# Kernel optimization log

Hardware: AMD Instinct MI355X
Metric: run time of the kernel (lower is better)

The kernel has to match this reference:

```python
import jax, jax.numpy as jnp
import numpy as np

MAX_FREQ = 4
OMEGA = 0.5 * np.pi
PATCH = 64


def _unnorm(c, size):
    # align_corners=False convention of torch.grid_sample
    return ((c + 1.0) * size - 1.0) / 2.0


def _gather(im, yy, xx):
    # im [C,H,W], yy/xx [Ho,Wo] -> [C,Ho,Wo]
    return im[:, yy, xx]


def _gs_nearest(inp, grid):
    # inp [B,C,H,W], grid [B,Ho,Wo,2] (x,y); padding_mode='border'
    B, C, H, W = inp.shape
    x = jnp.clip(jnp.round(_unnorm(grid[..., 0], W)), 0, W - 1).astype(jnp.int32)
    y = jnp.clip(jnp.round(_unnorm(grid[..., 1], H)), 0, H - 1).astype(jnp.int32)
    return jax.vmap(_gather)(inp, y, x)  # [B,C,Ho,Wo]


def _gs_bilinear(inp, grid):
    B, C, H, W = inp.shape
    x = jnp.clip(_unnorm(grid[..., 0], W), 0.0, W - 1.0)
    y = jnp.clip(_unnorm(grid[..., 1], H), 0.0, H - 1.0)
    x0 = jnp.floor(x); y0 = jnp.floor(y)
    wx = (x - x0)[:, None]; wy = (y - y0)[:, None]  # [B,1,Ho,Wo]
    x0i = x0.astype(jnp.int32); y0i = y0.astype(jnp.int32)
    x1i = jnp.minimum(x0i + 1, W - 1); y1i = jnp.minimum(y0i + 1, H - 1)
    g = jax.vmap(_gather)
    v00 = g(inp, y0i, x0i); v01 = g(inp, y0i, x1i)
    v10 = g(inp, y1i, x0i); v11 = g(inp, y1i, x1i)
    return (v00 * (1 - wx) * (1 - wy) + v01 * wx * (1 - wy)
            + v10 * (1 - wx) * wy + v11 * wx * wy)


def _conv2d(x, w, b):
    y = jax.lax.conv_general_dilated(x, w, (1, 1), ((1, 1), (1, 1)),
                                     dimension_numbers=("NCHW", "OIHW", "NCHW"))
    return y + b[None, :, None, None]


def _lc_decoder(q, rel):
    # q [B,Ho,Wo,2F+1], rel [B,Ho,Wo,1]; Fourier basis [1, cos(k*w*rel), sin(k*w*rel)]
    k = jnp.arange(1, MAX_FREQ + 1, dtype=q.dtype)
    ang = rel * k * OMEGA  # [B,Ho,Wo,F]
    basis = jnp.concatenate([jnp.ones_like(rel), jnp.cos(ang), jnp.sin(ang)], axis=-1)
    return jnp.sum(q * basis, axis=-1, keepdims=True)  # [B,Ho,Wo,1]


def _forward(sinogram, feat, grid, square_inv, adapt_w, adapt_b):
    B = feat.shape[0]
    sino = _conv2d(feat, adapt_w, adapt_b)          # [B,2F+1,V,D]
    V, D = sino.shape[-2], sino.shape[-1]
    # make_coord along detector axis (dim=1 coord channel), padding=0
    coord_d = ((jnp.arange(D, dtype=sino.dtype) + 0.5) / D) * 2.0 - 1.0
    sino_coord = jnp.broadcast_to(coord_d[None, None, None, :], (B, 1, V, D))
    shift_interval = 1.0 / D
    eps = 1e-4
    q_recons, lengths = [], []
    for sx in (-shift_interval, shift_interval):  # ensembling shifts
        g = grid + jnp.array([sx, 0.0], dtype=grid.dtype) + 1e-6
        q_recon = jnp.transpose(_gs_nearest(sino, g), (0, 2, 3, 1))       # [B,V,P2,2F+1]
        q_coord = jnp.transpose(_gs_nearest(sino_coord, g), (0, 2, 3, 1))  # [B,V,P2,1]
        rel = (grid[..., 0:1] - q_coord) * D
        q_recons.append(_lc_decoder(q_recon, rel))
        lengths.append(jnp.abs(rel) + eps)
    tot = lengths[0] + lengths[1]
    # lengths are swapped before weighting (cross weighting)
    recon = q_recons[0] * lengths[1] / tot + q_recons[1] * lengths[0] / tot
    out = jnp.sum(jnp.transpose(recon, (0, 3, 1, 2)) * square_inv * 10000.0, axis=-2)
    # back projection of center channel of raw sinogram
    ch = sinogram.shape[1]
    bp = _gs_bilinear(sinogram[:, ch // 2:ch // 2 + 1], grid)
    out = out + jnp.sum(bp * square_inv * 10000.0, axis=-2)  # [B,1,P2]
    return out.reshape(B, 1, PATCH, PATCH)


def setup_inputs() -> dict:
    key = jax.random.key(0)
    ks = jax.random.split(key, 6)
    B, V, D, ENC = 4, 360, 512, 64
    P2 = PATCH * PATCH
    CH = 2 * MAX_FREQ + 1
    return {
        "sinogram": jax.random.normal(ks[0], (B, 1, V, D), jnp.float32),
        "feat": jax.random.normal(ks[1], (B, ENC, V, D), jnp.float32),
        "grid": jax.random.uniform(ks[2], (B, V, P2, 2), jnp.float32, -1.0, 1.0),
        "square_inv": jax.random.uniform(ks[3], (B, 1, V, P2), jnp.float32, 1e-5, 1e-4),
        "adapt_w": jax.random.normal(ks[4], (CH, ENC, 3, 3), jnp.float32) * 0.05,
        "adapt_b": jax.random.normal(ks[5], (CH,), jnp.float32) * 0.05,
    }


def reference(sinogram, feat, grid, square_inv, adapt_w, adapt_b):
    return _forward(sinogram, feat, grid, square_inv, adapt_w, adapt_b)
```

## Files before the change

### kernel.cpp

```cpp
#include <hip/hip_runtime.h>
#include <hip/hip_fp16.h>
#include <math.h>

#define B   4
#define V   360
#define D   512
#define ENC 64
#define CH  9
#define P2  4096
#define NCHUNK 90
#define VCHUNK 4
#define RECH 16
#define PENT 513
#define PENTB 64

template <int PAIR>
__global__ __launch_bounds__(64) void conv_kernel(
    const float* __restrict__ feat,
    const float* __restrict__ w,
    const float* __restrict__ bias,
    char* __restrict__ outp)
{
    const int bid = blockIdx.x;
    const int sw  = (bid & 7) * 180 + (bid >> 3);
    const int b   = sw / V;
    const int v   = sw % V;
    const int d0  = threadIdx.x * 8;

    float acc[CH][8];
    #pragma unroll
    for (int oc = 0; oc < CH; ++oc) {
        const float bv = bias[oc];
        #pragma unroll
        for (int p = 0; p < 8; ++p) acc[oc][p] = bv;
    }

    const float* fb = feat + ((size_t)b * ENC * V + v) * D + d0;
    const bool vm = v > 0, vp = v < V - 1;
    const bool dm = d0 > 0, dp = d0 + 8 < D;

    float r0[3][10], r1[3][10];

    auto ld = [&](float r[3][10], int ic) {
        const float* f = fb + (size_t)ic * (V * D);
        #pragma unroll
        for (int rr = 0; rr < 3; ++rr) {
            const float* fr = f + (rr - 1) * D;
            const bool ok = (rr == 0) ? vm : ((rr == 2) ? vp : true);
            float4 c0 = ok ? *(const float4*)fr       : float4{0.f, 0.f, 0.f, 0.f};
            float4 c1 = ok ? *(const float4*)(fr + 4) : float4{0.f, 0.f, 0.f, 0.f};
            r[rr][1] = c0.x; r[rr][2] = c0.y; r[rr][3] = c0.z; r[rr][4] = c0.w;
            r[rr][5] = c1.x; r[rr][6] = c1.y; r[rr][7] = c1.z; r[rr][8] = c1.w;
            r[rr][0] = (ok && dm) ? fr[-1] : 0.f;
            r[rr][9] = (ok && dp) ? fr[8]  : 0.f;
        }
    };
    auto fmab = [&](const float r[3][10], int ic) {
        #pragma unroll
        for (int oc = 0; oc < CH; ++oc) {
            const float* ww = w + ((size_t)oc * ENC + ic) * 9;
            #pragma unroll
            for (int kr = 0; kr < 3; ++kr) {
                #pragma unroll
                for (int kc = 0; kc < 3; ++kc) {
                    const float wv = ww[kr * 3 + kc];
                    #pragma unroll
                    for (int p = 0; p < 8; ++p)
                        acc[oc][p] = fmaf(r[kr][p + kc], wv, acc[oc][p]);
                }
            }
        }
    };

    ld(r0, 0);
    #pragma unroll 1
    for (int ic = 0; ic < ENC; ic += 2) {
        ld(r1, ic + 1);
        fmab(r0, ic);
        if (ic + 2 < ENC) ld(r0, ic + 2);
        fmab(r1, ic + 1);
    }

    #pragma unroll
    for (int p = 0; p < 8; ++p) {
        union { __half2 h; unsigned u; } cv;
        uint4 pk;
        cv.h = __floats2half2_rn(acc[0][p], acc[1][p]); pk.x = cv.u;
        cv.h = __floats2half2_rn(acc[2][p], acc[3][p]); pk.y = cv.u;
        cv.h = __floats2half2_rn(acc[4][p], acc[5][p]); pk.z = cv.u;
        cv.h = __floats2half2_rn(acc[6][p], acc[7][p]); pk.w = cv.u;
        cv.h = __floats2half2_rn(acc[8][p], 0.f);
        const unsigned short z = (unsigned short)(cv.u & 0xffffu);
        const int x = d0 + p;
        if (PAIR) {
            char* row = outp + (size_t)(b * V + v) * PENT * PENTB;
            char* eA = row + (size_t)(x + 1) * PENTB;
            *(uint4*)eA = pk;
            *(unsigned short*)(eA + 32) = z;
            char* eB = row + (size_t)x * PENTB + 16;
            *(uint4*)eB = pk;
            *(unsigned short*)(eB + 18) = z;
            if (x == 0) {
                *(uint4*)row = pk;
                *(unsigned short*)(row + 32) = z;
            }
            if (x == D - 1) {
                char* eC = row + (size_t)512 * PENTB + 16;
                *(uint4*)eC = pk;
                *(unsigned short*)(eC + 18) = z;
            }
        } else {
            __half* rec = (__half*)outp + (size_t)(((size_t)b * V + v) * D + x) * RECH;
            *(uint4*)rec = pk;
            *(unsigned*)(rec + 8) = (unsigned)z;
        }
    }
}

__global__ __launch_bounds__(256) void build_sg4(
    const float* __restrict__ sg, float4* __restrict__ sg4)
{
    const int i  = blockIdx.x * 256 + threadIdx.x;
    const int x  = i & (D - 1);
    const int bv = i >> 9;
    const int v  = bv % V;
    const float a = sg[i];
    const float c = (x < D - 1) ? sg[i + 1] : a;
    const int i2 = (v < V - 1) ? i + D : i;
    const float d2 = sg[i2];
    const float e2 = (x < D - 1) ? sg[i2 + 1] : d2;
    sg4[i] = float4{a, c, d2, e2};
}

__global__ __launch_bounds__(256) void build_sg2(
    const float* __restrict__ sg, float2* __restrict__ sg2)
{
    const int i = blockIdx.x * 256 + threadIdx.x;
    const int x = i & (D - 1);
    const float a = sg[i];
    const float c = (x == D - 1) ? a : sg[i + 1];
    sg2[i] = float2{a, c};
}

__device__ __forceinline__ float decode_rec(uint4 a, unsigned short z, float rel)
{
    float q[9];
    union { unsigned uu; __half2 h; } c;
    float2 f;
    c.uu = a.x; f = __half22float2(c.h); q[0] = f.x; q[1] = f.y;
    c.uu = a.y; f = __half22float2(c.h); q[2] = f.x; q[3] = f.y;
    c.uu = a.z; f = __half22float2(c.h); q[4] = f.x; q[5] = f.y;
    c.uu = a.w; f = __half22float2(c.h); q[6] = f.x; q[7] = f.y;
    union { unsigned short us; __half hh; } c2;
    c2.us = z;
    q[8] = __half2float(c2.hh);

    const float ang = rel * 1.5707963267948966f;
    float s1, c1;
    __sincosf(ang, &s1, &c1);
    const float c2f = fmaf(2.f * c1, c1, -1.f);
    const float s2f = 2.f * c1 * s1;
    const float c3f = fmaf(2.f * c1, c2f, -c1);
    const float s3f = fmaf(2.f * c1, s2f, -s1);
    const float c4f = fmaf(2.f * c1, c3f, -c2f);
    const float s4f = fmaf(2.f * c1, s3f, -s2f);

    float vv = q[0];
    vv = fmaf(q[1], c1,  vv); vv = fmaf(q[2], c2f, vv);
    vv = fmaf(q[3], c3f, vv); vv = fmaf(q[4], c4f, vv);
    vv = fmaf(q[5], s1,  vv); vv = fmaf(q[6], s2f, vv);
    vv = fmaf(q[7], s3f, vv); vv = fmaf(q[8], s4f, vv);
    return vv;
}

template <int SG4>
__global__ __launch_bounds__(256) void sample_pair(
    const char* __restrict__ pair,
    const float4* __restrict__ sg4,
    const float2* __restrict__ sg2,
    const float* __restrict__ grid,
    const float* __restrict__ sq,
    float* __restrict__ partial)
{
    const int bid = blockIdx.x;
    const int xcd = bid & 7;
    const int b   = xcd >> 1;
    const int idx = ((bid >> 3) << 1) | (xcd & 1);
    const int chunk = idx >> 4;
    const int p  = (idx & 15) * 256 + threadIdx.x;
    const int v0 = chunk * VCHUNK;

    const char*   pb  = pair + (size_t)b * V * PENT * PENTB;
    const float4* s4b = sg4 + (size_t)b * V * D;
    const float2* s2b = sg2 + (size_t)b * V * D;

    float gx[4], gy[4], sv[4];
    #pragma unroll
    for (int u = 0; u < 4; ++u) {
        const size_t gi = (size_t)(b * V + v0 + u) * P2 + p;
        const double gd = __builtin_nontemporal_load((const double*)grid + gi);
        const unsigned long long gu = __double_as_longlong(gd);
        gx[u] = __uint_as_float((unsigned)gu);
        gy[u] = __uint_as_float((unsigned)(gu >> 32));
        sv[u] = __builtin_nontemporal_load(sq + gi);
    }

    uint4 qa[4], qb[4];
    unsigned short zA[4], zB[4];
    float relm[4], relp[4];
    #pragma unroll
    for (int u = 0; u < 4; ++u) {
        const float fy = ((gy[u] + 1e-6f + 1.f) * (float)V - 1.f) * 0.5f;
        const int   yi = (int)fminf(fmaxf(rintf(fy), 0.f), (float)(V - 1));
        const float fx0 = ((gx[u] + 1e-6f + 1.f) * (float)D - 1.f) * 0.5f;
        const int xm = (int)fminf(fmaxf(rintf(fx0 - 0.5f), 0.f), (float)(D - 1));
        const int xp = (int)fminf(fmaxf(rintf(fx0 + 0.5f), 0.f), (float)(D - 1));
        const float qcm = ((float)xm + 0.5f) * (2.f / (float)D) - 1.f;
        const float qcp = ((float)xp + 0.5f) * (2.f / (float)D) - 1.f;
        relm[u] = (gx[u] - qcm) * (float)D;
        relp[u] = (gx[u] - qcp) * (float)D;
        const char* rowp = pb + (size_t)yi * (PENT * PENTB);
        const char* e1 = rowp + (size_t)(xm + 1) * PENTB;
        const char* e2 = rowp + (size_t)xp * PENTB;
        qa[u] = *(const uint4*)e1;
        qb[u] = *(const uint4*)(e2 + 16);
        const unsigned zab = *(const unsigned*)(e1 + 32);
        zA[u] = (unsigned short)(zab & 0xffffu);
        zB[u] = (e2 == e1) ? (unsigned short)(zab >> 16)
                           : *(const unsigned short*)(e2 + 34);
    }

    float bl00[4], bl01[4], bl10[4], bl11[4], wxv[4], wyv[4];
    #pragma unroll
    for (int u = 0; u < 4; ++u) {
        float fxb = fminf(fmaxf(((gx[u] + 1.f) * (float)D - 1.f) * 0.5f, 0.f), (float)(D - 1));
        float fyb = fminf(fmaxf(((gy[u] + 1.f) * (float)V - 1.f) * 0.5f, 0.f), (float)(V - 1));
        const float x0 = floorf(fxb), y0 = floorf(fyb);
        wxv[u] = fxb - x0; wyv[u] = fyb - y0;
        const int x0i = (int)x0, y0i = (int)y0;
        if (SG4) {
            const float4 t = s4b[y0i * D + x0i];
            bl00[u] = t.x; bl01[u] = t.y; bl10[u] = t.z; bl11[u] = t.w;
        } else {
            const int y1i = min(y0i + 1, V - 1);
            const float2 t  = s2b[y0i * D + x0i];
            const float2 u2 = s2b[y1i * D + x0i];
            bl00[u] = t.x;  bl01[u] = t.y;
            bl10[u] = u2.x; bl11[u] = u2.y;
        }
    }

    __builtin_amdgcn_sched_barrier(0);

    float acc = 0.f;
    #pragma unroll
    for (int u = 0; u < 4; ++u) {
        const float vmv = decode_rec(qa[u], zA[u], relm[u]);
        const float vpv = decode_rec(qb[u], zB[u], relp[u]);
        const float lm = fabsf(relm[u]) + 1e-4f;
        const float lp = fabsf(relp[u]) + 1e-4f;
        const float recon = (vmv * lp + vpv * lm) / (lm + lp);

        const float wx = wxv[u], wy = wyv[u];
        const float bp = bl00[u] * (1.f - wx) * (1.f - wy) + bl01[u] * wx * (1.f - wy)
                       + bl10[u] * (1.f - wx) * wy         + bl11[u] * wx * wy;

        acc += (recon + bp) * sv[u] * 1e4f;
    }
    __builtin_nontemporal_store(acc, partial + ((size_t)chunk * B + b) * P2 + p);
}

template <int PAIRED>
__global__ __launch_bounds__(256) void sample_basic(
    const __half* __restrict__ sino,
    const float* __restrict__ sinogram,
    const float2* __restrict__ sg2,
    const float* __restrict__ grid,
    const float* __restrict__ sq,
    float* __restrict__ partial)
{
    const int bid = blockIdx.x;
    const int xcd = bid & 7;
    const int b   = xcd >> 1;
    const int idx = ((bid >> 3) << 1) | (xcd & 1);
    const int chunk = idx >> 4;
    const int p  = (idx & 15) * 256 + threadIdx.x;
    const int v0 = chunk * VCHUNK;

    const float*  sg   = sinogram + (size_t)b * V * D;
    const float2* s2b  = sg2 + (size_t)b * V * D;
    const __half* sb   = sino + (size_t)b * V * D * RECH;

    float gx[4], gy[4], sv[4];
    #pragma unroll
    for (int u = 0; u < 4; ++u) {
        const size_t gi = (size_t)(b * V + v0 + u) * P2 + p;
        const double gd = __builtin_nontemporal_load((const double*)grid + gi);
        const unsigned long long gu = __double_as_longlong(gd);
        gx[u] = __uint_as_float((unsigned)gu);
        gy[u] = __uint_as_float((unsigned)(gu >> 32));
        sv[u] = __builtin_nontemporal_load(sq + gi);
    }

    uint4    ra[4][2];
    unsigned rz[4][2];
    float    rel[4][2];
    #pragma unroll
    for (int u = 0; u < 4; ++u) {
        const float fy = ((gy[u] + 1e-6f + 1.f) * (float)V - 1.f) * 0.5f;
        const int   yi = (int)fminf(fmaxf(rintf(fy), 0.f), (float)(V - 1));
        const float fx0 = ((gx[u] + 1e-6f + 1.f) * (float)D - 1.f) * 0.5f;
        #pragma unroll
        for (int sft = 0; sft < 2; ++sft) {
            const float fx = (sft == 0) ? (fx0 - 0.5f) : (fx0 + 0.5f);
            const int   xi = (int)fminf(fmaxf(rintf(fx), 0.f), (float)(D - 1));
            const float qc = ((float)xi + 0.5f) * (2.f / (float)D) - 1.f;
            rel[u][sft] = (gx[u] - qc) * (float)D;
            const __half* rec = sb + (size_t)(yi * D + xi) * RECH;
            ra[u][sft] = *(const uint4*)rec;
            rz[u][sft] = *(const unsigned*)(rec + 8);
        }
    }

    float bl00[4], bl01[4], bl10[4], bl11[4], wxv[4], wyv[4];
    #pragma unroll
    for (int u = 0; u < 4; ++u) {
        float fxb = fminf(fmaxf(((gx[u] + 1.f) * (float)D - 1.f) * 0.5f, 0.f), (float)(D - 1));
        float fyb = fminf(fmaxf(((gy[u] + 1.f) * (float)V - 1.f) * 0.5f, 0.f), (float)(V - 1));
        const float x0 = floorf(fxb), y0 = floorf(fyb);
        wxv[u] = fxb - x0; wyv[u] = fyb - y0;
        const int x0i = (int)x0, y0i = (int)y0;
        const int y1i = min(y0i + 1, V - 1);
        if (PAIRED) {
            const float2 t  = s2b[y0i * D + x0i];
            const float2 u2 = s2b[y1i * D + x0i];
            bl00[u] = t.x;  bl01[u] = t.y;
            bl10[u] = u2.x; bl11[u] = u2.y;
        } else {
            const int x1i = min(x0i + 1, D - 1);
            bl00[u] = sg[y0i * D + x0i]; bl01[u] = sg[y0i * D + x1i];
            bl10[u] = sg[y1i * D + x0i]; bl11[u] = sg[y1i * D + x1i];
        }
    }

    __builtin_amdgcn_sched_barrier(0);

    float acc = 0.f;
    #pragma unroll
    for (int u = 0; u < 4; ++u) {
        const float v0f = decode_rec(ra[u][0], (unsigned short)(rz[u][0] & 0xffffu), rel[u][0]);
        const float v1f = decode_rec(ra[u][1], (unsigned short)(rz[u][1] & 0xffffu), rel[u][1]);
        const float l0 = fabsf(rel[u][0]) + 1e-4f;
        const float l1 = fabsf(rel[u][1]) + 1e-4f;
        const float recon = (v0f * l1 + v1f * l0) / (l0 + l1);
        const float wx = wxv[u], wy = wyv[u];
        const float bp = bl00[u] * (1.f - wx) * (1.f - wy) + bl01[u] * wx * (1.f - wy)
                       + bl10[u] * (1.f - wx) * wy         + bl11[u] * wx * wy;
        acc += (recon + bp) * sv[u] * 1e4f;
    }
    __builtin_nontemporal_store(acc, partial + ((size_t)chunk * B + b) * P2 + p);
}

__global__ __launch_bounds__(256) void reduce_kernel(
    const float* __restrict__ partial, float* __restrict__ out)
{
    const int i = blockIdx.x * 256 + threadIdx.x;
    float a = 0.f;
    #pragma unroll 6
    for (int c = 0; c < NCHUNK; ++c)
        a += __builtin_nontemporal_load(partial + (size_t)c * B * P2 + i);
    out[i] = a;
}

extern "C" void kernel_launch(void* const* d_in, const int* in_sizes, int n_in,
                              void* d_out, int out_size, void* d_ws, size_t ws_size,
                              hipStream_t stream)
{
    const float* sinogram = (const float*)d_in[0];
    const float* feat     = (const float*)d_in[1];
    const float* grid     = (const float*)d_in[2];
    const float* sq       = (const float*)d_in[3];
    const float* w        = (const float*)d_in[4];
    const float* bias     = (const float*)d_in[5];
    float* out = (float*)d_out;

    const size_t pair_b = (size_t)B * V * PENT * PENTB;
    const size_t part_b = (size_t)NCHUNK * B * P2 * sizeof(float);
    const size_t sg4_b  = (size_t)B * V * D * sizeof(float4);
    const size_t sg2_b  = (size_t)B * V * D * sizeof(float2);
    const size_t rec_b  = (size_t)B * V * D * RECH * sizeof(__half);

    if (ws_size >= pair_b + part_b + sg4_b) {
        char*   pair    = (char*)d_ws;
        float*  partial = (float*)((char*)d_ws + pair_b);
        float4* sg4     = (float4*)((char*)d_ws + pair_b + part_b);
        conv_kernel<1><<<dim3(1440), 64, 0, stream>>>(feat, w, bias, pair);
        build_sg4<<<dim3(2880), 256, 0, stream>>>(sinogram, sg4);
        sample_pair<1><<<dim3(5760), 256, 0, stream>>>(pair, sg4, (const float2*)sg4, grid, sq, partial);
        reduce_kernel<<<dim3((B * P2) / 256), 256, 0, stream>>>(partial, out);
    } else if (ws_size >= pair_b + part_b + sg2_b) {
        char*   pair    = (char*)d_ws;
        float*  partial = (float*)((char*)d_ws + pair_b);
        float2* sg2     = (float2*)((char*)d_ws + pair_b + part_b);
        conv_kernel<1><<<dim3(1440), 64, 0, stream>>>(feat, w, bias, pair);
        build_sg2<<<dim3(2880), 256, 0, stream>>>(sinogram, sg2);
        sample_pair<0><<<dim3(5760), 256, 0, stream>>>(pair, (const float4*)sg2, sg2, grid, sq, partial);
        reduce_kernel<<<dim3((B * P2) / 256), 256, 0, stream>>>(partial, out);
    } else if (ws_size >= rec_b + part_b + sg2_b) {
        char*   sino    = (char*)d_ws;
        float*  partial = (float*)((char*)d_ws + rec_b);
        float2* sg2     = (float2*)((char*)d_ws + rec_b + part_b);
        conv_kernel<0><<<dim3(1440), 64, 0, stream>>>(feat, w, bias, sino);
        build_sg2<<<dim3(2880), 256, 0, stream>>>(sinogram, sg2);
        sample_basic<1><<<dim3(5760), 256, 0, stream>>>((const __half*)sino, sinogram, sg2, grid, sq, partial);
        reduce_kernel<<<dim3((B * P2) / 256), 256, 0, stream>>>(partial, out);
    } else {
        char*   sino    = (char*)d_ws;
        float*  partial = (float*)((char*)d_ws + rec_b);
        conv_kernel<0><<<dim3(1440), 64, 0, stream>>>(feat, w, bias, sino);
        sample_basic<0><<<dim3(5760), 256, 0, stream>>>((const __half*)sino, sinogram, (const float2*)sino, grid, sq, partial);
        reduce_kernel<<<dim3((B * P2) / 256), 256, 0, stream>>>(partial, out);
    }
}
```

Before: 330.1 us.

## Use packed fp16 dot2 for conv with prepacked half2 weights and larger blocks

Converts the 3x3 conv inner loop from fp32 FMAs to v_dot2 on half2 pairs of input channels, and adds a small kernel that packs the weights into half2 per channel pair. Blocks grow from 64 to 256 threads covering four view rows, and the grid shrinks to match. The aim is to halve the conv's FMA instruction count. In exchange it loses precision on the inputs and weights, drops the software double-buffered loads, and adds one extra kernel launch.

```diff
diff --git a/kernel.cpp b/kernel.cpp
--- a/kernel.cpp
+++ b/kernel.cpp
@@ -13,19 +13,55 @@
 #define RECH 16
 #define PENT 513
 #define PENTB 64
+#define NIC2 (ENC / 2)
+#define WPN  (NIC2 * CH * 9)
+
+typedef _Float16 hp2 __attribute__((ext_vector_type(2)));
+
+__device__ __forceinline__ float dot2f(unsigned a, unsigned b, float c)
+{
+#if __has_builtin(__builtin_amdgcn_fdot2)
+    return __builtin_amdgcn_fdot2(__builtin_bit_cast(hp2, a),
+                                  __builtin_bit_cast(hp2, b), c, false);
+#else
+    union { unsigned u; __half2 h; } ua, ub;
+    ua.u = a; ub.u = b;
+    const float2 fa = __half22float2(ua.h);
+    const float2 fb = __half22float2(ub.h);
+    return fmaf(fa.y, fb.y, fmaf(fa.x, fb.x, c));
+#endif
+}
+
+__global__ __launch_bounds__(256) void pack_weights(
+    const float* __restrict__ w, unsigned* __restrict__ wp)
+{
+    const int i = blockIdx.x * 256 + threadIdx.x;
+    if (i >= WPN) return;
+    const int ic2 = i / (CH * 9);
+    const int r   = i - ic2 * (CH * 9);
+    const int oc  = r / 9;
+    const int k   = r - oc * 9;
+    const float a = w[((size_t)oc * ENC + 2 * ic2) * 9 + k];
+    const float b = w[((size_t)oc * ENC + 2 * ic2 + 1) * 9 + k];
+    union { __half2 h; unsigned u; } cv;
+    cv.h = __floats2half2_rn(a, b);
+    wp[i] = cv.u;
+}
 
 template <int PAIR>
-__global__ __launch_bounds__(64) void conv_kernel(
+__global__ __launch_bounds__(256) void conv_kernel(
     const float* __restrict__ feat,
-    const float* __restrict__ w,
+    const unsigned* __restrict__ wp,
     const float* __restrict__ bias,
     char* __restrict__ outp)
 {
     const int bid = blockIdx.x;
-    const int sw  = (bid & 7) * 180 + (bid >> 3);
-    const int b   = sw / V;
-    const int v   = sw % V;
-    const int d0  = threadIdx.x * 8;
+    const int sw  = (bid & 7) * 45 + (bid >> 3);
+    const int b   = sw / 90;
+    const int vt  = sw % 90;
+    const int tr  = threadIdx.x >> 6;
+    const int v   = vt * 4 + tr;
+    const int d0  = (threadIdx.x & 63) * 8;
 
     float acc[CH][8];
     #pragma unroll
@@ -39,46 +75,50 @@
     const bool vm = v > 0, vp = v < V - 1;
     const bool dm = d0 > 0, dp = d0 + 8 < D;
 
-    float r0[3][10], r1[3][10];
-
-    auto ld = [&](float r[3][10], int ic) {
-        const float* f = fb + (size_t)ic * (V * D);
+    #pragma unroll 1
+    for (int ic2 = 0; ic2 < NIC2; ++ic2) {
+        float rA[3][10], rB[3][10];
         #pragma unroll
-        for (int rr = 0; rr < 3; ++rr) {
-            const float* fr = f + (rr - 1) * D;
-            const bool ok = (rr == 0) ? vm : ((rr == 2) ? vp : true);
-            float4 c0 = ok ? *(const float4*)fr       : float4{0.f, 0.f, 0.f, 0.f};
-            float4 c1 = ok ? *(const float4*)(fr + 4) : float4{0.f, 0.f, 0.f, 0.f};
-            r[rr][1] = c0.x; r[rr][2] = c0.y; r[rr][3] = c0.z; r[rr][4] = c0.w;
-            r[rr][5] = c1.x; r[rr][6] = c1.y; r[rr][7] = c1.z; r[rr][8] = c1.w;
-            r[rr][0] = (ok && dm) ? fr[-1] : 0.f;
-            r[rr][9] = (ok && dp) ? fr[8]  : 0.f;
-        }
-    };
-    auto fmab = [&](const float r[3][10], int ic) {
+        for (int half = 0; half < 2; ++half) {
+            float (*r)[10] = half ? rB : rA;
+            const float* f = fb + (size_t)(2 * ic2 + half) * (V * D);
+            #pragma unroll
+            for (int rr = 0; rr < 3; ++rr) {
+                const float* fr = f + (rr - 1) * D;
+                const bool ok = (rr == 0) ? vm : ((rr == 2) ? vp : true);
+                float4 c0 = ok ? *(const float4*)fr       : float4{0.f, 0.f, 0.f, 0.f};
+                float4 c1 = ok ? *(const float4*)(fr + 4) : float4{0.f, 0.f, 0.f, 0.f};
+                r[rr][1] = c0.x; r[rr][2] = c0.y; r[rr][3] = c0.z; r[rr][4] = c0.w;
+                r[rr][5] = c1.x; r[rr][6] = c1.y; r[rr][7] = c1.z; r[rr][8] = c1.w;
+                r[rr][0] = (ok && dm) ? fr[-1] : 0.f;
+                r[rr][9] = (ok && dp) ? fr[8]  : 0.f;
+            }
+        }
+        unsigned pv[3][10];
+        #pragma unroll
+        for (int rr = 0; rr < 3; ++rr)
+            #pragma unroll
+            for (int t = 0; t < 10; ++t) {
+                union { __half2 h; unsigned u; } cv;
+                cv.h = __floats2half2_rn(rA[rr][t], rB[rr][t]);
+                pv[rr][t] = cv.u;
+            }
+
+        const unsigned* wbase = wp + ic2 * (CH * 9);
         #pragma unroll
         for (int oc = 0; oc < CH; ++oc) {
-            const float* ww = w + ((size_t)oc * ENC + ic) * 9;
+            const unsigned* ww = wbase + oc * 9;
             #pragma unroll
             for (int kr = 0; kr < 3; ++kr) {
                 #pragma unroll
                 for (int kc = 0; kc < 3; ++kc) {
-                    const float wv = ww[kr * 3 + kc];
+                    const unsigned wv = ww[kr * 3 + kc];
                     #pragma unroll
                     for (int p = 0; p < 8; ++p)
-                        acc[oc][p] = fmaf(r[kr][p + kc], wv, acc[oc][p]);
+                        acc[oc][p] = dot2f(pv[kr][p + kc], wv, acc[oc][p]);
                 }
             }
         }
-    };
-
-    ld(r0, 0);
-    #pragma unroll 1
-    for (int ic = 0; ic < ENC; ic += 2) {
-        ld(r1, ic + 1);
-        fmab(r0, ic);
-        if (ic + 2 < ENC) ld(r0, ic + 2);
-        fmab(r1, ic + 1);
     }
 
     #pragma unroll
@@ -389,35 +429,44 @@
     const size_t sg4_b  = (size_t)B * V * D * sizeof(float4);
     const size_t sg2_b  = (size_t)B * V * D * sizeof(float2);
     const size_t rec_b  = (size_t)B * V * D * RECH * sizeof(__half);
-
-    if (ws_size >= pair_b + part_b + sg4_b) {
-        char*   pair    = (char*)d_ws;
-        float*  partial = (float*)((char*)d_ws + pair_b);
-        float4* sg4     = (float4*)((char*)d_ws + pair_b + part_b);
-        conv_kernel<1><<<dim3(1440), 64, 0, stream>>>(feat, w, bias, pair);
+    const size_t wp_b   = (size_t)WPN * sizeof(unsigned);
+
+    if (ws_size >= pair_b + part_b + sg4_b + wp_b) {
+        char*     pair    = (char*)d_ws;
+        float*    partial = (float*)((char*)d_ws + pair_b);
+        float4*   sg4     = (float4*)((char*)d_ws + pair_b + part_b);
+        unsigned* wpp     = (unsigned*)((char*)d_ws + pair_b + part_b + sg4_b);
+        pack_weights<<<dim3((WPN + 255) / 256), 256, 0, stream>>>(w, wpp);
+        conv_kernel<1><<<dim3(360), 256, 0, stream>>>(feat, wpp, bias, pair);
         build_sg4<<<dim3(2880), 256, 0, stream>>>(sinogram, sg4);
         sample_pair<1><<<dim3(5760), 256, 0, stream>>>(pair, sg4, (const float2*)sg4, grid, sq, partial);
         reduce_kernel<<<dim3((B * P2) / 256), 256, 0, stream>>>(partial, out);
-    } else if (ws_size >= pair_b + part_b + sg2_b) {
-        char*   pair    = (char*)d_ws;
-        float*  partial = (float*)((char*)d_ws + pair_b);
-        float2* sg2     = (float2*)((char*)d_ws + pair_b + part_b);
-        conv_kernel<1><<<dim3(1440), 64, 0, stream>>>(feat, w, bias, pair);
+    } else if (ws_size >= pair_b + part_b + sg2_b + wp_b) {
+        char*     pair    = (char*)d_ws;
+        float*    partial = (float*)((char*)d_ws + pair_b);
+        float2*   sg2     = (float2*)((char*)d_ws + pair_b + part_b);
+        unsigned* wpp     = (unsigned*)((char*)d_ws + pair_b + part_b + sg2_b);
+        pack_weights<<<dim3((WPN + 255) / 256), 256, 0, stream>>>(w, wpp);
+        conv_kernel<1><<<dim3(360), 256, 0, stream>>>(feat, wpp, bias, pair);
         build_sg2<<<dim3(2880), 256, 0, stream>>>(sinogram, sg2);
         sample_pair<0><<<dim3(5760), 256, 0, stream>>>(pair, (const float4*)sg2, sg2, grid, sq, partial);
         reduce_kernel<<<dim3((B * P2) / 256), 256, 0, stream>>>(partial, out);
-    } else if (ws_size >= rec_b + part_b + sg2_b) {
-        char*   sino    = (char*)d_ws;
-        float*  partial = (float*)((char*)d_ws + rec_b);
-        float2* sg2     = (float2*)((char*)d_ws + rec_b + part_b);
-        conv_kernel<0><<<dim3(1440), 64, 0, stream>>>(feat, w, bias, sino);
+    } else if (ws_size >= rec_b + part_b + sg2_b + wp_b) {
+        char*     sino    = (char*)d_ws;
+        float*    partial = (float*)((char*)d_ws + rec_b);
+        float2*   sg2     = (float2*)((char*)d_ws + rec_b + part_b);
+        unsigned* wpp     = (unsigned*)((char*)d_ws + rec_b + part_b + sg2_b);
+        pack_weights<<<dim3((WPN + 255) / 256), 256, 0, stream>>>(w, wpp);
+        conv_kernel<0><<<dim3(360), 256, 0, stream>>>(feat, wpp, bias, sino);
         build_sg2<<<dim3(2880), 256, 0, stream>>>(sinogram, sg2);
         sample_basic<1><<<dim3(5760), 256, 0, stream>>>((const __half*)sino, sinogram, sg2, grid, sq, partial);
         reduce_kernel<<<dim3((B * P2) / 256), 256, 0, stream>>>(partial, out);
     } else {
-        char*   sino    = (char*)d_ws;
-        float*  partial = (float*)((char*)d_ws + rec_b);
-        conv_kernel<0><<<dim3(1440), 64, 0, stream>>>(feat, w, bias, sino);
+        char*     sino    = (char*)d_ws;
+        float*    partial = (float*)((char*)d_ws + rec_b);
+        unsigned* wpp     = (unsigned*)((char*)d_ws + rec_b + part_b);
+        pack_weights<<<dim3((WPN + 255) / 256), 256, 0, stream>>>(w, wpp);
+        conv_kernel<0><<<dim3(360), 256, 0, stream>>>(feat, wpp, bias, sino);
         sample_basic<0><<<dim3(5760), 256, 0, stream>>>((const __half*)sino, sinogram, (const float2*)sino, grid, sq, partial);
         reduce_kernel<<<dim3((B * P2) / 256), 256, 0, stream>>>(partial, out);
     }
```

New measurement: 354.6 us. +7.4%, slower.

## Split conv over input-channel halves with a combine pass, use 256-thread blocks

Applied to the files above, without the earlier changes.

The 3x3 adapter conv is split across two halves of the input channels. Each half writes fp32 partial sums to a new workspace buffer, and a separate combine kernel adds them and packs the fp16 pair layout. Conv blocks grow from 64 to 256 threads covering four rows, and the manual double-buffered load loop is replaced by a simple loop. The aim is more parallelism and occupancy in the conv, paid for by an extra kernel launch and a round trip of about 26MB of partials through memory. The split path needs a larger workspace; otherwise it falls back to the single-pass conv.

```diff
diff --git a/kernel.cpp b/kernel.cpp
--- a/kernel.cpp
+++ b/kernel.cpp
@@ -13,19 +13,152 @@
 #define RECH 16
 #define PENT 513
 #define PENTB 64
+#define NPX (B * V * D)
+
+typedef float vfloat4 __attribute__((ext_vector_type(4)));
+
+__device__ __forceinline__ void ld_rows8(
+    float r[3][10], const float* f, bool vm, bool vp, bool dm, bool dp)
+{
+    #pragma unroll
+    for (int rr = 0; rr < 3; ++rr) {
+        const float* fr = f + (rr - 1) * D;
+        const bool ok = (rr == 0) ? vm : ((rr == 2) ? vp : true);
+        float4 c0 = ok ? *(const float4*)fr       : float4{0.f, 0.f, 0.f, 0.f};
+        float4 c1 = ok ? *(const float4*)(fr + 4) : float4{0.f, 0.f, 0.f, 0.f};
+        r[rr][1] = c0.x; r[rr][2] = c0.y; r[rr][3] = c0.z; r[rr][4] = c0.w;
+        r[rr][5] = c1.x; r[rr][6] = c1.y; r[rr][7] = c1.z; r[rr][8] = c1.w;
+        r[rr][0] = (ok && dm) ? fr[-1] : 0.f;
+        r[rr][9] = (ok && dp) ? fr[8]  : 0.f;
+    }
+}
+
+__device__ __forceinline__ void fma_block8(
+    float acc[CH][8], const float r[3][10], const float* __restrict__ w, int ic)
+{
+    #pragma unroll
+    for (int oc = 0; oc < CH; ++oc) {
+        const float* ww = w + ((size_t)oc * ENC + ic) * 9;
+        #pragma unroll
+        for (int kr = 0; kr < 3; ++kr) {
+            #pragma unroll
+            for (int kc = 0; kc < 3; ++kc) {
+                const float wv = ww[kr * 3 + kc];
+                #pragma unroll
+                for (int p = 0; p < 8; ++p)
+                    acc[oc][p] = fmaf(r[kr][p + kc], wv, acc[oc][p]);
+            }
+        }
+    }
+}
+
+__global__ __launch_bounds__(256) void conv_split(
+    const float* __restrict__ feat,
+    const float* __restrict__ w,
+    const float* __restrict__ bias,
+    float* __restrict__ cp)
+{
+    const int bid = blockIdx.x;
+    const int sw  = (bid & 7) * 90 + (bid >> 3);
+    const int half = sw / 360;
+    const int rem  = sw - half * 360;
+    const int b  = rem / 90;
+    const int vt = rem % 90;
+    const int tr = threadIdx.x >> 6;
+    const int v  = vt * 4 + tr;
+    const int d0 = (threadIdx.x & 63) * 8;
+    const int ic0 = half * (ENC / 2);
+
+    float acc[CH][8];
+    #pragma unroll
+    for (int oc = 0; oc < CH; ++oc) {
+        const float bv = half ? 0.f : bias[oc];
+        #pragma unroll
+        for (int p = 0; p < 8; ++p) acc[oc][p] = bv;
+    }
+
+    const float* fb = feat + ((size_t)b * ENC * V + v) * D + d0;
+    const bool vm = v > 0, vp = v < V - 1;
+    const bool dm = d0 > 0, dp = d0 + 8 < D;
+
+    for (int ic = ic0; ic < ic0 + ENC / 2; ++ic) {
+        float r[3][10];
+        ld_rows8(r, fb + (size_t)ic * (V * D), vm, vp, dm, dp);
+        fma_block8(acc, r, w, ic);
+    }
+
+    const size_t rowb = ((size_t)b * V + v) * D + d0;
+    #pragma unroll
+    for (int ch = 0; ch < CH; ++ch) {
+        float* dst = cp + (size_t)(half * CH + ch) * NPX + rowb;
+        vfloat4 v0 = {acc[ch][0], acc[ch][1], acc[ch][2], acc[ch][3]};
+        vfloat4 v1 = {acc[ch][4], acc[ch][5], acc[ch][6], acc[ch][7]};
+        __builtin_nontemporal_store(v0, (vfloat4*)dst);
+        __builtin_nontemporal_store(v1, (vfloat4*)(dst + 4));
+    }
+}
 
 template <int PAIR>
-__global__ __launch_bounds__(64) void conv_kernel(
+__global__ __launch_bounds__(256) void combine_kernel(
+    const float* __restrict__ cp, char* __restrict__ outp)
+{
+    const int id = blockIdx.x * 256 + threadIdx.x;
+    const int x  = id & (D - 1);
+    const int bv = id >> 9;
+
+    float q[9];
+    #pragma unroll
+    for (int ch = 0; ch < CH; ++ch)
+        q[ch] = __builtin_nontemporal_load(cp + (size_t)ch * NPX + id)
+              + __builtin_nontemporal_load(cp + (size_t)(CH + ch) * NPX + id);
+
+    union { __half2 h; unsigned u; } cv;
+    uint4 pk;
+    cv.h = __floats2half2_rn(q[0], q[1]); pk.x = cv.u;
+    cv.h = __floats2half2_rn(q[2], q[3]); pk.y = cv.u;
+    cv.h = __floats2half2_rn(q[4], q[5]); pk.z = cv.u;
+    cv.h = __floats2half2_rn(q[6], q[7]); pk.w = cv.u;
+    cv.h = __floats2half2_rn(q[8], 0.f);
+    const unsigned short z = (unsigned short)(cv.u & 0xffffu);
+
+    if (PAIR) {
+        char* row = outp + (size_t)bv * PENT * PENTB;
+        char* eA = row + (size_t)(x + 1) * PENTB;
+        *(uint4*)eA = pk;
+        *(unsigned short*)(eA + 32) = z;
+        char* eB = row + (size_t)x * PENTB + 16;
+        *(uint4*)eB = pk;
+        *(unsigned short*)(eB + 18) = z;
+        if (x == 0) {
+            *(uint4*)row = pk;
+            *(unsigned short*)(row + 32) = z;
+        }
+        if (x == D - 1) {
+            char* eC = row + (size_t)512 * PENTB + 16;
+            *(uint4*)eC = pk;
+            *(unsigned short*)(eC + 18) = z;
+        }
+    } else {
+        __half* rec = (__half*)outp + (size_t)id * RECH;
+        *(uint4*)rec = pk;
+        *(unsigned*)(rec + 8) = (unsigned)z;
+    }
+}
+
+template <int PAIR>
+__global__ __launch_bounds__(256) void conv_mono(
     const float* __restrict__ feat,
     const float* __restrict__ w,
     const float* __restrict__ bias,
     char* __restrict__ outp)
 {
     const int bid = blockIdx.x;
-    const int sw  = (bid & 7) * 180 + (bid >> 3);
-    const int b   = sw / V;
-    const int v   = sw % V;
-    const int d0  = threadIdx.x * 8;
+    const int sw  = (bid & 7) * 45 + (bid >> 3);
+    const int b   = sw / 90;
+    const int vt  = sw % 90;
+    const int tr  = threadIdx.x >> 6;
+    const int v   = vt * 4 + tr;
+    const int d0  = (threadIdx.x & 63) * 8;
 
     float acc[CH][8];
     #pragma unroll
@@ -39,46 +172,10 @@
     const bool vm = v > 0, vp = v < V - 1;
     const bool dm = d0 > 0, dp = d0 + 8 < D;
 
-    float r0[3][10], r1[3][10];
-
-    auto ld = [&](float r[3][10], int ic) {
-        const float* f = fb + (size_t)ic * (V * D);
-        #pragma unroll
-        for (int rr = 0; rr < 3; ++rr) {
-            const float* fr = f + (rr - 1) * D;
-            const bool ok = (rr == 0) ? vm : ((rr == 2) ? vp : true);
-            float4 c0 = ok ? *(const float4*)fr       : float4{0.f, 0.f, 0.f, 0.f};
-            float4 c1 = ok ? *(const float4*)(fr + 4) : float4{0.f, 0.f, 0.f, 0.f};
-            r[rr][1] = c0.x; r[rr][2] = c0.y; r[rr][3] = c0.z; r[rr][4] = c0.w;
-            r[rr][5] = c1.x; r[rr][6] = c1.y; r[rr][7] = c1.z; r[rr][8] = c1.w;
-            r[rr][0] = (ok && dm) ? fr[-1] : 0.f;
-            r[rr][9] = (ok && dp) ? fr[8]  : 0.f;
-        }
-    };
-    auto fmab = [&](const float r[3][10], int ic) {
-        #pragma unroll
-        for (int oc = 0; oc < CH; ++oc) {
-            const float* ww = w + ((size_t)oc * ENC + ic) * 9;
-            #pragma unroll
-            for (int kr = 0; kr < 3; ++kr) {
-                #pragma unroll
-                for (int kc = 0; kc < 3; ++kc) {
-                    const float wv = ww[kr * 3 + kc];
-                    #pragma unroll
-                    for (int p = 0; p < 8; ++p)
-                        acc[oc][p] = fmaf(r[kr][p + kc], wv, acc[oc][p]);
-                }
-            }
-        }
-    };
-
-    ld(r0, 0);
-    #pragma unroll 1
-    for (int ic = 0; ic < ENC; ic += 2) {
-        ld(r1, ic + 1);
-        fmab(r0, ic);
-        if (ic + 2 < ENC) ld(r0, ic + 2);
-        fmab(r1, ic + 1);
+    for (int ic = 0; ic < ENC; ++ic) {
+        float r[3][10];
+        ld_rows8(r, fb + (size_t)ic * (V * D), vm, vp, dm, dp);
+        fma_block8(acc, r, w, ic);
     }
 
     #pragma unroll
@@ -389,12 +486,23 @@
     const size_t sg4_b  = (size_t)B * V * D * sizeof(float4);
     const size_t sg2_b  = (size_t)B * V * D * sizeof(float2);
     const size_t rec_b  = (size_t)B * V * D * RECH * sizeof(__half);
-
-    if (ws_size >= pair_b + part_b + sg4_b) {
+    const size_t cp_b   = (size_t)2 * CH * NPX * sizeof(float);
+
+    if (ws_size >= pair_b + part_b + sg4_b + cp_b) {
         char*   pair    = (char*)d_ws;
         float*  partial = (float*)((char*)d_ws + pair_b);
         float4* sg4     = (float4*)((char*)d_ws + pair_b + part_b);
-        conv_kernel<1><<<dim3(1440), 64, 0, stream>>>(feat, w, bias, pair);
+        float*  cp      = (float*)((char*)d_ws + pair_b + part_b + sg4_b);
+        conv_split<<<dim3(720), 256, 0, stream>>>(feat, w, bias, cp);
+        build_sg4<<<dim3(2880), 256, 0, stream>>>(sinogram, sg4);
+        combine_kernel<1><<<dim3(2880), 256, 0, stream>>>(cp, pair);
+        sample_pair<1><<<dim3(5760), 256, 0, stream>>>(pair, sg4, (const float2*)sg4, grid, sq, partial);
+        reduce_kernel<<<dim3((B * P2) / 256), 256, 0, stream>>>(partial, out);
+    } else if (ws_size >= pair_b + part_b + sg4_b) {
+        char*   pair    = (char*)d_ws;
+        float*  partial = (float*)((char*)d_ws + pair_b);
+        float4* sg4     = (float4*)((char*)d_ws + pair_b + part_b);
+        conv_mono<1><<<dim3(360), 256, 0, stream>>>(feat, w, bias, pair);
         build_sg4<<<dim3(2880), 256, 0, stream>>>(sinogram, sg4);
         sample_pair<1><<<dim3(5760), 256, 0, stream>>>(pair, sg4, (const float2*)sg4, grid, sq, partial);
         reduce_kernel<<<dim3((B * P2) / 256), 256, 0, stream>>>(partial, out);
@@ -402,7 +510,7 @@
         char*   pair    = (char*)d_ws;
         float*  partial = (float*)((char*)d_ws + pair_b);
         float2* sg2     = (float2*)((char*)d_ws + pair_b + part_b);
-        conv_kernel<1><<<dim3(1440), 64, 0, stream>>>(feat, w, bias, pair);
+        conv_mono<1><<<dim3(360), 256, 0, stream>>>(feat, w, bias, pair);
         build_sg2<<<dim3(2880), 256, 0, stream>>>(sinogram, sg2);
         sample_pair<0><<<dim3(5760), 256, 0, stream>>>(pair, (const float4*)sg2, sg2, grid, sq, partial);
         reduce_kernel<<<dim3((B * P2) / 256), 256, 0, stream>>>(partial, out);
@@ -410,14 +518,14 @@
         char*   sino    = (char*)d_ws;
         float*  partial = (float*)((char*)d_ws + rec_b);
         float2* sg2     = (float2*)((char*)d_ws + rec_b + part_b);
-        conv_kernel<0><<<dim3(1440), 64, 0, stream>>>(feat, w, bias, sino);
+        conv_mono<0><<<dim3(360), 256, 0, stream>>>(feat, w, bias, sino);
         build_sg2<<<dim3(2880), 256, 0, stream>>>(sinogram, sg2);
         sample_basic<1><<<dim3(5760), 256, 0, stream>>>((const __half*)sino, sinogram, sg2, grid, sq, partial);
         reduce_kernel<<<dim3((B * P2) / 256), 256, 0, stream>>>(partial, out);
     } else {
         char*   sino    = (char*)d_ws;
         float*  partial = (float*)((char*)d_ws + rec_b);
-        conv_kernel<0><<<dim3(1440), 64, 0, stream>>>(feat, w, bias, sino);
+        conv_mono<0><<<dim3(360), 256, 0, stream>>>(feat, w, bias, sino);
         sample_basic<0><<<dim3(5760), 256, 0, stream>>>((const __half*)sino, sinogram, (const float2*)sino, grid, sq, partial);
         reduce_kernel<<<dim3((B * P2) / 256), 256, 0, stream>>>(partial, out);
     }
```

After: 289.8 us. 12.2% less time.
